# Kernel tuning notes

Measured on AMD Instinct MI355X. Metric: run time of the kernel, lower is better.

The kernel has to match this reference:

```python
import jax, jax.numpy as jnp
import numpy as np

EMBED_DIM = 1024
NUM_HEADS = 16
HEAD_DIM = EMBED_DIM // NUM_HEADS
SCALING = HEAD_DIM ** -0.5
TGT_LEN, BSZ = 2048, 2


def setup_inputs() -> dict:
    key = jax.random.key(0)
    k1, k2, k3 = jax.random.split(key, 3)
    return {
        "query": jax.random.normal(k1, (TGT_LEN, BSZ, EMBED_DIM), jnp.float32),
        "in_proj_weight": jax.random.normal(k2, (3 * EMBED_DIM, EMBED_DIM), jnp.float32) * (EMBED_DIM ** -0.5),
        "in_proj_bias": jnp.zeros((3 * EMBED_DIM,), jnp.float32),
        "out_w": jax.random.normal(k3, (EMBED_DIM, EMBED_DIM), jnp.float32) * (EMBED_DIM ** -0.5),
        "out_b": jnp.zeros((EMBED_DIM,), jnp.float32),
    }


def reference(query, in_proj_weight, in_proj_bias, out_w, out_b):
    tgt_len, bsz, embed_dim = query.shape
    # fused QKV projection (self-attention path: qkv_same)
    qkv = query @ in_proj_weight.T + in_proj_bias  # [T, B, 3E]
    q, k, v = jnp.split(qkv, 3, axis=-1)
    q = q * SCALING
    # [T, B, E] -> [B*H, T, hd]
    def to_heads(x):
        return x.reshape(tgt_len, bsz * NUM_HEADS, HEAD_DIM).transpose(1, 0, 2)
    q, k, v = to_heads(q), to_heads(k), to_heads(v)
    attn_weights = jnp.einsum('bqd,bkd->bqk', q, k)          # [B*H, T, T]
    attn_weights = jax.nn.softmax(attn_weights, axis=-1)
    attn = jnp.einsum('bqk,bkd->bqd', attn_weights, v)       # [B*H, T, hd]
    attn = attn.transpose(1, 0, 2).reshape(tgt_len, bsz, embed_dim)
    attn = attn @ out_w.T + out_b
    # averaged attention weights over heads (need_weights=True)
    avg_weights = attn_weights.reshape(bsz, NUM_HEADS, tgt_len, tgt_len).mean(axis=1)
    return attn, avg_weights
```

## Files before the change

### kernel.cpp

```cpp
#include <hip/hip_runtime.h>
#include <hip/hip_bf16.h>
#include <math.h>

#define T_LEN 2048
#define BSZ   2
#define EMB   1024
#define NH    16
#define HD    64
#define BHN   (BSZ*NH)
#define M1    (T_LEN*BSZ)
#define SCAL  0.125f
#define QSCALE (0.125f * 1.44269504088896f)

typedef __attribute__((ext_vector_type(8))) short bf16x8;
typedef __attribute__((ext_vector_type(4))) float f32x4;
typedef __attribute__((ext_vector_type(2))) unsigned int u32x2;

__device__ inline unsigned short f2bf(float x) {
    union { float f; unsigned u; } v; v.f = x;
    unsigned r = v.u + 0x7FFF + ((v.u >> 16) & 1);
    return (unsigned short)(r >> 16);
}

__device__ inline unsigned pack2bf(float a, float b) {
    union { __hip_bfloat162 h; unsigned u; } v;
    v.h = __float22bfloat162_rn(make_float2(a, b));
    return v.u;
}

__device__ inline float fexp2(float x) {
#if __has_builtin(__builtin_amdgcn_exp2f)
    return __builtin_amdgcn_exp2f(x);
#else
    return exp2f(x);
#endif
}

__device__ inline void async16(const unsigned short* g, unsigned short* l) {
    __builtin_amdgcn_global_load_lds(
        (const __attribute__((address_space(1))) void*)g,
        (__attribute__((address_space(3))) void*)l, 16, 0, 0);
}

__device__ inline void bar() {
    asm volatile("" ::: "memory");
    __builtin_amdgcn_s_barrier();
    asm volatile("" ::: "memory");
}

__device__ inline const unsigned short* swz(const unsigned short* base, int r, int c) {
    return base + (((r << 3) + (c ^ (r & 7))) << 3);
}
__device__ inline const unsigned short* swz16(const unsigned short* base, int r, int c) {
    return base + (((r << 4) + (c ^ (r & 7))) << 3);
}

__device__ inline void xchg(unsigned e, unsigned o, unsigned& w_lo, unsigned& w_hi) {
#if __has_builtin(__builtin_amdgcn_permlane32_swap) && __has_builtin(__builtin_amdgcn_permlane16_swap)
    u32x2 x = __builtin_amdgcn_permlane32_swap(e, o, false, false);
    u32x2 y = __builtin_amdgcn_permlane16_swap(x[0], x[1], false, false);
    w_lo = y[0]; w_hi = y[1];
#else
    int lane = (int)(threadIdx.x & 63);
    int quad = lane >> 4, l16 = lane & 15;
    int srcA = ((quad & 1) * 2) * 16 + l16;
    int srcB = ((quad & 1) * 2 + 1) * 16 + l16;
    unsigned ea = (unsigned)__shfl((int)e, srcA, 64);
    unsigned oa = (unsigned)__shfl((int)o, srcA, 64);
    unsigned eb = (unsigned)__shfl((int)e, srcB, 64);
    unsigned ob = (unsigned)__shfl((int)o, srcB, 64);
    w_lo = (quad >> 1) ? oa : ea;
    w_hi = (quad >> 1) ? ob : eb;
#endif
}

__global__ __launch_bounds__(256) void cvt3_kernel(
    const float* __restrict__ s0, const float* __restrict__ s1,
    const float* __restrict__ s2, unsigned short* __restrict__ dst,
    int n0, int n1)
{
    int idx = blockIdx.x * 256 + threadIdx.x;
    const float* src; int o;
    if (idx < n0)           { src = s0; o = idx; }
    else if (idx < n0 + n1) { src = s1; o = idx - n0; }
    else                    { src = s2; o = idx - n0 - n1; }
    float4 a = reinterpret_cast<const float4*>(src)[(size_t)o * 2];
    float4 c = reinterpret_cast<const float4*>(src)[(size_t)o * 2 + 1];
    unsigned w[4] = { pack2bf(a.x, a.y), pack2bf(a.z, a.w),
                      pack2bf(c.x, c.y), pack2bf(c.z, c.w) };
    reinterpret_cast<uint4*>(dst)[idx] = *reinterpret_cast<uint4*>(w);
}

__global__ __launch_bounds__(256) void qkv_mfma_kernel(
    const unsigned short* __restrict__ A, const unsigned short* __restrict__ B,
    const float* __restrict__ bias,
    unsigned short* __restrict__ Q16, unsigned short* __restrict__ K16,
    unsigned short* __restrict__ Vt16)
{
    constexpr int BM = 128, BN = 128, BK = 32, K = 1024;
    __shared__ unsigned short As[BM * BK];
    __shared__ unsigned short Bs[BN * BK];
    const int tid = threadIdx.x;
    const int lane = tid & 63, wave = tid >> 6;
    const int quad = lane >> 4, l16 = lane & 15;
    const int wr = wave >> 1, wc = wave & 1;
    const int m0 = blockIdx.x * BM, n0 = blockIdx.y * BN;

    f32x4 zero4 = {0.f, 0.f, 0.f, 0.f};
    f32x4 acc[4][4];
    #pragma unroll
    for (int i = 0; i < 4; ++i)
        #pragma unroll
        for (int j = 0; j < 4; ++j) acc[i][j] = zero4;

    for (int k0 = 0; k0 < K; k0 += BK) {
        __syncthreads();
        #pragma unroll
        for (int t = 0; t < 2; ++t) {
            int c = t * 256 + tid;
            int m = c >> 2, kb = c & 3;
            async16(&A[(size_t)(m0 + m) * K + k0 + kb * 8], &As[c * 8]);
            async16(&B[(size_t)(n0 + m) * K + k0 + kb * 8], &Bs[c * 8]);
        }
        __syncthreads();
        bf16x8 af[4], bfr[4];
        #pragma unroll
        for (int i = 0; i < 4; ++i) {
            af[i]  = *reinterpret_cast<const bf16x8*>(&As[(wr * 64 + i * 16 + l16) * BK + quad * 8]);
            bfr[i] = *reinterpret_cast<const bf16x8*>(&Bs[(wc * 64 + i * 16 + l16) * BK + quad * 8]);
        }
        #pragma unroll
        for (int i = 0; i < 4; ++i)
            #pragma unroll
            for (int j = 0; j < 4; ++j)
                acc[i][j] = __builtin_amdgcn_mfma_f32_16x16x32_bf16(af[i], bfr[j], acc[i][j], 0, 0, 0);
    }

    #pragma unroll
    for (int j = 0; j < 4; ++j) {
        int n = n0 + wc * 64 + j * 16 + l16;
        float bv = bias[n];
        int which = n >> 10;
        int c = n & 1023;
        int h = c >> 6, d = c & 63;
        #pragma unroll
        for (int i = 0; i < 4; ++i) {
            #pragma unroll
            for (int r = 0; r < 4; ++r) {
                int m = m0 + wr * 64 + i * 16 + quad * 4 + r;
                int t = m >> 1, b = m & 1;
                int bh = b * NH + h;
                float v = acc[i][j][r] + bv;
                if (which == 0)      Q16[((size_t)bh * T_LEN + t) * HD + d] = f2bf(v * QSCALE);
                else if (which == 1) K16[((size_t)bh * T_LEN + t) * HD + d] = f2bf(v);
                else                 Vt16[((size_t)bh * HD + d) * T_LEN + t] = f2bf(v);
            }
        }
    }
}

__global__ __launch_bounds__(512, 4) void flash_mfma_kernel(
    const unsigned short* __restrict__ Qb, const unsigned short* __restrict__ Kb,
    const unsigned short* __restrict__ Vt, unsigned short* __restrict__ AO,
    float* __restrict__ Rrow)
{
    __shared__ unsigned short Ks[2][128 * 64];
    __shared__ unsigned short Vs[2][64 * 128];
    const int tid = threadIdx.x;
    const int lane = tid & 63, wave = tid >> 6;
    const int quad = lane >> 4, l16 = lane & 15;

    const int lin = blockIdx.y * gridDim.x + blockIdx.x;
    const int xcd = lin & 7, slot = lin >> 3;
    const int bh = xcd * 4 + (slot >> 4);
    const int qt = slot & 15;
    const int q0 = qt * 128;
    const int b = bh >> 4, h = bh & 15;

    const unsigned short* Qp =
        Qb + ((size_t)bh * T_LEN + q0 + wave * 16 + l16) * HD;
    bf16x8 qf0 = *reinterpret_cast<const bf16x8*>(Qp + quad * 8);
    bf16x8 qf1 = *reinterpret_cast<const bf16x8*>(Qp + 32 + quad * 8);

    f32x4 zero4 = {0.f, 0.f, 0.f, 0.f};
    f32x4 oacc[4] = {zero4, zero4, zero4, zero4};
    float l_part = 0.f;

    const unsigned short* Kbase = Kb + (size_t)bh * T_LEN * HD;
    const unsigned short* Vbase = Vt + (size_t)bh * HD * T_LEN;

    const int ck0 = tid, ck1 = tid + 512;
    const int kr0 = ck0 >> 3, kc0 = (ck0 & 7) ^ (kr0 & 7);
    const int kr1 = ck1 >> 3, kc1 = (ck1 & 7) ^ (kr1 & 7);
    const int vr0 = ck0 >> 4, vc0 = (ck0 & 15) ^ (vr0 & 7);
    const int vr1 = ck1 >> 4, vc1 = (ck1 & 15) ^ (vr1 & 7);

    auto stage = [&](int buf, int kt) {
        async16(&Kbase[(size_t)(kt + kr0) * HD + kc0 * 8], &Ks[buf][ck0 * 8]);
        async16(&Kbase[(size_t)(kt + kr1) * HD + kc1 * 8], &Ks[buf][ck1 * 8]);
        async16(&Vbase[(size_t)vr0 * T_LEN + kt + vc0 * 8], &Vs[buf][ck0 * 8]);
        async16(&Vbase[(size_t)vr1 * T_LEN + kt + vc1 * 8], &Vs[buf][ck1 * 8]);
    };

    stage(0, 0);

    int cur = 0;
    for (int kt = 0; kt < T_LEN; kt += 128) {
        if (kt + 128 < T_LEN) {
            stage(cur ^ 1, kt + 128);
            asm volatile("s_waitcnt vmcnt(4)" ::: "memory");
        } else {
            asm volatile("s_waitcnt vmcnt(0)" ::: "memory");
        }
        bar();

        const unsigned short* Kt = Ks[cur];
        const unsigned short* Vv = Vs[cur];

        unsigned dlo[8], dhi[8];
        #pragma unroll
        for (int half = 0; half < 2; ++half) {
            f32x4 sacc[4] = {zero4, zero4, zero4, zero4};
            __builtin_amdgcn_s_setprio(1);
            #pragma unroll
            for (int j = 0; j < 4; ++j) {
                int kb = half * 4 + j;
                bf16x8 kf0 = *reinterpret_cast<const bf16x8*>(swz(Kt, kb * 16 + l16, quad));
                sacc[j] = __builtin_amdgcn_mfma_f32_16x16x32_bf16(kf0, qf0, sacc[j], 0, 0, 0);
                bf16x8 kf1 = *reinterpret_cast<const bf16x8*>(swz(Kt, kb * 16 + l16, 4 + quad));
                sacc[j] = __builtin_amdgcn_mfma_f32_16x16x32_bf16(kf1, qf1, sacc[j], 0, 0, 0);
            }
            __builtin_amdgcn_s_setprio(0);
            #pragma unroll
            for (int j = 0; j < 4; ++j) {
                float p0 = fexp2(sacc[j][0]);
                float p1 = fexp2(sacc[j][1]);
                float p2 = fexp2(sacc[j][2]);
                float p3 = fexp2(sacc[j][3]);
                l_part += (p0 + p1) + (p2 + p3);
                dlo[half * 4 + j] = pack2bf(p0, p1);
                dhi[half * 4 + j] = pack2bf(p2, p3);
            }
        }

        __builtin_amdgcn_s_setprio(1);
        #pragma unroll
        for (int ks = 0; ks < 4; ++ks) {
            unsigned w0, w1, w2, w3;
            xchg(dlo[2 * ks], dlo[2 * ks + 1], w0, w2);
            xchg(dhi[2 * ks], dhi[2 * ks + 1], w1, w3);
            union { bf16x8 v; unsigned u[4]; } P;
            P.u[0] = w0; P.u[1] = w1; P.u[2] = w2; P.u[3] = w3;
            #pragma unroll
            for (int dt = 0; dt < 4; ++dt) {
                bf16x8 va = *reinterpret_cast<const bf16x8*>(swz16(Vv, dt * 16 + l16, ks * 4 + quad));
                oacc[dt] = __builtin_amdgcn_mfma_f32_16x16x32_bf16(va, P.v, oacc[dt], 0, 0, 0);
            }
        }
        __builtin_amdgcn_s_setprio(0);

        bar();
        cur ^= 1;
    }

    l_part += __shfl_xor(l_part, 16);
    l_part += __shfl_xor(l_part, 32);
    float rl = 1.0f / l_part;
    int q = q0 + wave * 16 + l16;
    size_t base = ((size_t)q * BSZ + b) * EMB + h * HD;
    #pragma unroll
    for (int dt = 0; dt < 4; ++dt) {
        unsigned o[2] = { pack2bf(oacc[dt][0] * rl, oacc[dt][1] * rl),
                          pack2bf(oacc[dt][2] * rl, oacc[dt][3] * rl) };
        *reinterpret_cast<uint2*>(&AO[base + dt * 16 + quad * 4]) = *reinterpret_cast<uint2*>(o);
    }
    if (quad == 0)
        Rrow[(size_t)bh * T_LEN + q] = rl;
}

__global__ __launch_bounds__(256) void avg_mfma_kernel(
    const unsigned short* __restrict__ Qb, const unsigned short* __restrict__ Kb,
    const float* __restrict__ Rrow, float* __restrict__ avg_out)
{
    __shared__ unsigned short Ks[2][2][64 * 64];
    const int tid = threadIdx.x;
    const int lane = tid & 63, wave = tid >> 6;
    const int quad = lane >> 4, l16 = lane & 15;
    const int kt = blockIdx.x, qt = blockIdx.y, b = blockIdx.z;
    const int q0 = qt * 128, k0 = kt * 64;

    auto stage_pair = [&](int buf, int h0) {
        const unsigned short* Kg = Kb + ((size_t)(b * NH + h0) * T_LEN + k0) * HD;
        #pragma unroll
        for (int t = 0; t < 4; ++t) {
            int c = t * 256 + tid;
            int hh = c >> 9, cl = c & 511;
            int r = cl >> 3, cc = (cl & 7) ^ (r & 7);
            async16(&Kg[(size_t)hh * T_LEN * HD + (size_t)r * HD + cc * 8],
                    &Ks[buf][0][0] + (size_t)c * 8);
        }
    };

    f32x4 zero4 = {0.f, 0.f, 0.f, 0.f};
    f32x4 acc[2][4];
    #pragma unroll
    for (int s = 0; s < 2; ++s)
        #pragma unroll
        for (int c = 0; c < 4; ++c) acc[s][c] = zero4;

    stage_pair(0, 0);
    int cur = 0;
    for (int g = 0; g < NH / 2; ++g) {
        if (g + 1 < NH / 2) {
            stage_pair(cur ^ 1, 2 * (g + 1));
            asm volatile("s_waitcnt vmcnt(4)" ::: "memory");
        } else {
            asm volatile("s_waitcnt vmcnt(0)" ::: "memory");
        }
        bar();

        #pragma unroll
        for (int hh = 0; hh < 2; ++hh) {
            const int bh = b * NH + 2 * g + hh;
            const unsigned short* Kt = Ks[cur][hh];
            bf16x8 kf[4][2];
            #pragma unroll
            for (int c = 0; c < 4; ++c) {
                kf[c][0] = *reinterpret_cast<const bf16x8*>(swz(Kt, c * 16 + l16, quad));
                kf[c][1] = *reinterpret_cast<const bf16x8*>(swz(Kt, c * 16 + l16, 4 + quad));
            }
            #pragma unroll
            for (int s = 0; s < 2; ++s) {
                const int qrow = q0 + s * 64 + wave * 16;
                const unsigned short* Qp = Qb + ((size_t)bh * T_LEN + qrow + l16) * HD;
                bf16x8 qf0 = *reinterpret_cast<const bf16x8*>(Qp + quad * 8);
                bf16x8 qf1 = *reinterpret_cast<const bf16x8*>(Qp + 32 + quad * 8);
                float4 rlv = *reinterpret_cast<const float4*>(
                    &Rrow[(size_t)bh * T_LEN + qrow + quad * 4]);

                f32x4 sacc[4] = {zero4, zero4, zero4, zero4};
                __builtin_amdgcn_s_setprio(1);
                #pragma unroll
                for (int c = 0; c < 4; ++c) {
                    sacc[c] = __builtin_amdgcn_mfma_f32_16x16x32_bf16(qf0, kf[c][0], sacc[c], 0, 0, 0);
                    sacc[c] = __builtin_amdgcn_mfma_f32_16x16x32_bf16(qf1, kf[c][1], sacc[c], 0, 0, 0);
                }
                __builtin_amdgcn_s_setprio(0);

                float rl4[4] = { rlv.x, rlv.y, rlv.z, rlv.w };
                #pragma unroll
                for (int c = 0; c < 4; ++c)
                    #pragma unroll
                    for (int r = 0; r < 4; ++r)
                        acc[s][c][r] += fexp2(sacc[c][r]) * rl4[r];
            }
        }
        bar();
        cur ^= 1;
    }

    #pragma unroll
    for (int s = 0; s < 2; ++s)
        #pragma unroll
        for (int r = 0; r < 4; ++r) {
            int q = q0 + s * 64 + wave * 16 + quad * 4 + r;
            size_t base = ((size_t)b * T_LEN + q) * T_LEN + k0;
            #pragma unroll
            for (int c = 0; c < 4; ++c)
                avg_out[base + c * 16 + l16] = acc[s][c][r] * (1.0f / 16.0f);
        }
}

__global__ __launch_bounds__(256) void out_mfma_kernel(
    const unsigned short* __restrict__ A, const unsigned short* __restrict__ B,
    const float* __restrict__ bias, float* __restrict__ out)
{
    constexpr int BM = 128, BN = 128, BK = 32, K = 1024;
    __shared__ unsigned short As[BM * BK];
    __shared__ unsigned short Bs[BN * BK];
    const int tid = threadIdx.x;
    const int lane = tid & 63, wave = tid >> 6;
    const int quad = lane >> 4, l16 = lane & 15;
    const int wr = wave >> 1, wc = wave & 1;
    const int m0 = blockIdx.x * BM, n0 = blockIdx.y * BN;

    f32x4 zero4 = {0.f, 0.f, 0.f, 0.f};
    f32x4 acc[4][4];
    #pragma unroll
    for (int i = 0; i < 4; ++i)
        #pragma unroll
        for (int j = 0; j < 4; ++j) acc[i][j] = zero4;

    for (int k0 = 0; k0 < K; k0 += BK) {
        __syncthreads();
        #pragma unroll
        for (int t = 0; t < 2; ++t) {
            int c = t * 256 + tid;
            int m = c >> 2, kb = c & 3;
            async16(&A[(size_t)(m0 + m) * K + k0 + kb * 8], &As[c * 8]);
            async16(&B[(size_t)(n0 + m) * K + k0 + kb * 8], &Bs[c * 8]);
        }
        __syncthreads();
        bf16x8 af[4], bfr[4];
        #pragma unroll
        for (int i = 0; i < 4; ++i) {
            af[i]  = *reinterpret_cast<const bf16x8*>(&As[(wr * 64 + i * 16 + l16) * BK + quad * 8]);
            bfr[i] = *reinterpret_cast<const bf16x8*>(&Bs[(wc * 64 + i * 16 + l16) * BK + quad * 8]);
        }
        #pragma unroll
        for (int i = 0; i < 4; ++i)
            #pragma unroll
            for (int j = 0; j < 4; ++j)
                acc[i][j] = __builtin_amdgcn_mfma_f32_16x16x32_bf16(af[i], bfr[j], acc[i][j], 0, 0, 0);
    }

    #pragma unroll
    for (int j = 0; j < 4; ++j) {
        int n = n0 + wc * 64 + j * 16 + l16;
        float bv = bias[n];
        #pragma unroll
        for (int i = 0; i < 4; ++i) {
            #pragma unroll
            for (int r = 0; r < 4; ++r) {
                int m = m0 + wr * 64 + i * 16 + quad * 4 + r;
                out[(size_t)m * 1024 + n] = acc[i][j][r] + bv;
            }
        }
    }
}

extern "C" void kernel_launch(void* const* d_in, const int* in_sizes, int n_in,
                              void* d_out, int out_size, void* d_ws, size_t ws_size,
                              hipStream_t stream)
{
    const float* query = (const float*)d_in[0];
    const float* wqkv  = (const float*)d_in[1];
    const float* bqkv  = (const float*)d_in[2];
    const float* wout  = (const float*)d_in[3];
    const float* bout  = (const float*)d_in[4];
    float* out = (float*)d_out;

    char* ws = (char*)d_ws;
    const size_t E_Q   = (size_t)M1 * EMB;
    const size_t E_W   = (size_t)3 * EMB * EMB;
    const size_t E_WO  = (size_t)EMB * EMB;
    const size_t E_QKV = (size_t)BHN * T_LEN * HD;

    unsigned short* queryb = (unsigned short*)ws;
    unsigned short* wqkvb  = queryb + E_Q;
    unsigned short* woutb  = wqkvb + E_W;
    unsigned short* Q16    = woutb + E_WO;
    unsigned short* K16    = Q16 + E_QKV;
    unsigned short* Vt16   = K16 + E_QKV;
    unsigned short* AO16   = Vt16 + E_QKV;
    float* Lr = (float*)(AO16 + E_Q);
    const size_t need = (E_Q + E_W + E_WO + 4 * E_QKV) * 2 + (size_t)BHN * T_LEN * 4;
    if (ws_size < need) return;

    cvt3_kernel<<<(int)((E_Q + E_W + E_WO) / 8 / 256), 256, 0, stream>>>(
        query, wqkv, wout, queryb, (int)(E_Q / 8), (int)(E_W / 8));

    qkv_mfma_kernel<<<dim3(M1 / 128, 3072 / 128), 256, 0, stream>>>(queryb, wqkvb, bqkv, Q16, K16, Vt16);
    flash_mfma_kernel<<<dim3(T_LEN / 128, BHN), 512, 0, stream>>>(Q16, K16, Vt16, AO16, Lr);
    avg_mfma_kernel<<<dim3(T_LEN / 64, T_LEN / 128, BSZ), 256, 0, stream>>>(Q16, K16, Lr, out + (size_t)M1 * EMB);
    out_mfma_kernel<<<dim3(M1 / 128, 1024 / 128), 256, 0, stream>>>(AO16, woutb, bout, out);
}
```

Measured before the change: 240.6 us.

## Load K fragments directly to registers in avg kernel, dropping LDS staging

The head-averaged attention-weights kernel no longer stages K tiles through shared memory with async copies and barriers. Each wave now loads its K MFMA fragments straight from global memory into registers, double-buffered in registers across heads so the next head's load overlaps the current head's compute. This removes LDS traffic and block-wide synchronisation, but every wave now fetches the same K data redundantly from global/L2, and register pressure rises from the two fragment buffers.

```diff
diff --git a/kernel.cpp b/kernel.cpp
--- a/kernel.cpp
+++ b/kernel.cpp
@@ -282,25 +282,12 @@
     const unsigned short* __restrict__ Qb, const unsigned short* __restrict__ Kb,
     const float* __restrict__ Rrow, float* __restrict__ avg_out)
 {
-    __shared__ unsigned short Ks[2][2][64 * 64];
     const int tid = threadIdx.x;
     const int lane = tid & 63, wave = tid >> 6;
     const int quad = lane >> 4, l16 = lane & 15;
     const int kt = blockIdx.x, qt = blockIdx.y, b = blockIdx.z;
     const int q0 = qt * 128, k0 = kt * 64;
 
-    auto stage_pair = [&](int buf, int h0) {
-        const unsigned short* Kg = Kb + ((size_t)(b * NH + h0) * T_LEN + k0) * HD;
-        #pragma unroll
-        for (int t = 0; t < 4; ++t) {
-            int c = t * 256 + tid;
-            int hh = c >> 9, cl = c & 511;
-            int r = cl >> 3, cc = (cl & 7) ^ (r & 7);
-            async16(&Kg[(size_t)hh * T_LEN * HD + (size_t)r * HD + cc * 8],
-                    &Ks[buf][0][0] + (size_t)c * 8);
-        }
-    };
-
     f32x4 zero4 = {0.f, 0.f, 0.f, 0.f};
     f32x4 acc[2][4];
     #pragma unroll
@@ -308,55 +295,56 @@
         #pragma unroll
         for (int c = 0; c < 4; ++c) acc[s][c] = zero4;
 
-    stage_pair(0, 0);
-    int cur = 0;
+    const unsigned short* Kl =
+        Kb + ((size_t)(b * NH) * T_LEN + k0 + l16) * HD + quad * 8;
+
+    auto loadK = [&](bf16x8 (&kf)[4][2], int h) {
+        const unsigned short* p = Kl + (size_t)h * T_LEN * HD;
+        #pragma unroll
+        for (int c = 0; c < 4; ++c) {
+            kf[c][0] = *reinterpret_cast<const bf16x8*>(p + (size_t)c * 16 * HD);
+            kf[c][1] = *reinterpret_cast<const bf16x8*>(p + (size_t)c * 16 * HD + 32);
+        }
+    };
+
+    auto compute = [&](bf16x8 (&kf)[4][2], int h) {
+        const int bh = b * NH + h;
+        #pragma unroll
+        for (int s = 0; s < 2; ++s) {
+            const int qrow = q0 + s * 64 + wave * 16;
+            const unsigned short* Qp = Qb + ((size_t)bh * T_LEN + qrow + l16) * HD;
+            bf16x8 qf0 = *reinterpret_cast<const bf16x8*>(Qp + quad * 8);
+            bf16x8 qf1 = *reinterpret_cast<const bf16x8*>(Qp + 32 + quad * 8);
+            float4 rlv = *reinterpret_cast<const float4*>(
+                &Rrow[(size_t)bh * T_LEN + qrow + quad * 4]);
+
+            f32x4 sacc[4] = {zero4, zero4, zero4, zero4};
+            __builtin_amdgcn_s_setprio(1);
+            #pragma unroll
+            for (int c = 0; c < 4; ++c) {
+                sacc[c] = __builtin_amdgcn_mfma_f32_16x16x32_bf16(qf0, kf[c][0], sacc[c], 0, 0, 0);
+                sacc[c] = __builtin_amdgcn_mfma_f32_16x16x32_bf16(qf1, kf[c][1], sacc[c], 0, 0, 0);
+            }
+            __builtin_amdgcn_s_setprio(0);
+
+            float rl4[4] = { rlv.x, rlv.y, rlv.z, rlv.w };
+            #pragma unroll
+            for (int c = 0; c < 4; ++c)
+                #pragma unroll
+                for (int r = 0; r < 4; ++r)
+                    acc[s][c][r] += fexp2(sacc[c][r]) * rl4[r];
+        }
+    };
+
+    bf16x8 kfA[4][2], kfB[4][2];
+    loadK(kfA, 0);
+    #pragma unroll
     for (int g = 0; g < NH / 2; ++g) {
-        if (g + 1 < NH / 2) {
-            stage_pair(cur ^ 1, 2 * (g + 1));
-            asm volatile("s_waitcnt vmcnt(4)" ::: "memory");
-        } else {
-            asm volatile("s_waitcnt vmcnt(0)" ::: "memory");
-        }
-        bar();
-
-        #pragma unroll
-        for (int hh = 0; hh < 2; ++hh) {
-            const int bh = b * NH + 2 * g + hh;
-            const unsigned short* Kt = Ks[cur][hh];
-            bf16x8 kf[4][2];
-            #pragma unroll
-            for (int c = 0; c < 4; ++c) {
-                kf[c][0] = *reinterpret_cast<const bf16x8*>(swz(Kt, c * 16 + l16, quad));
-                kf[c][1] = *reinterpret_cast<const bf16x8*>(swz(Kt, c * 16 + l16, 4 + quad));
-            }
-            #pragma unroll
-            for (int s = 0; s < 2; ++s) {
-                const int qrow = q0 + s * 64 + wave * 16;
-                const unsigned short* Qp = Qb + ((size_t)bh * T_LEN + qrow + l16) * HD;
-                bf16x8 qf0 = *reinterpret_cast<const bf16x8*>(Qp + quad * 8);
-                bf16x8 qf1 = *reinterpret_cast<const bf16x8*>(Qp + 32 + quad * 8);
-                float4 rlv = *reinterpret_cast<const float4*>(
-                    &Rrow[(size_t)bh * T_LEN + qrow + quad * 4]);
-
-                f32x4 sacc[4] = {zero4, zero4, zero4, zero4};
-                __builtin_amdgcn_s_setprio(1);
-                #pragma unroll
-                for (int c = 0; c < 4; ++c) {
-                    sacc[c] = __builtin_amdgcn_mfma_f32_16x16x32_bf16(qf0, kf[c][0], sacc[c], 0, 0, 0);
-                    sacc[c] = __builtin_amdgcn_mfma_f32_16x16x32_bf16(qf1, kf[c][1], sacc[c], 0, 0, 0);
-                }
-                __builtin_amdgcn_s_setprio(0);
-
-                float rl4[4] = { rlv.x, rlv.y, rlv.z, rlv.w };
-                #pragma unroll
-                for (int c = 0; c < 4; ++c)
-                    #pragma unroll
-                    for (int r = 0; r < 4; ++r)
-                        acc[s][c][r] += fexp2(sacc[c][r]) * rl4[r];
-            }
-        }
-        bar();
-        cur ^= 1;
+        loadK(kfB, 2 * g + 1);
+        compute(kfA, 2 * g);
+        if (2 * g + 2 < NH)
+            loadK(kfA, 2 * g + 2);
+        compute(kfB, 2 * g + 1);
     }
 
     #pragma unroll
```

After: 333.0 us. +38.4%, slower.

## Merge averaged-weights and output-projection kernels into one interleaved launch

Applied to the files above, without the earlier changes.

Combines the head-averaged attention weight kernel and the output projection GEMM into a single launch of 1280 blocks, where every fifth block runs a GEMM tile and the rest run avg tiles, sharing one shared-memory buffer. This removes one kernel launch and the tail/idle gap between the two kernels, letting the compute-heavy GEMM tiles overlap with the store-heavy avg tiles. The cost is a larger register and shared-memory footprint taken as the maximum of both paths, which may lower occupancy, plus block-level divergence in scheduling.

```diff
diff --git a/kernel.cpp b/kernel.cpp
--- a/kernel.cpp
+++ b/kernel.cpp
@@ -278,154 +278,153 @@
         Rrow[(size_t)bh * T_LEN + q] = rl;
 }
 
-__global__ __launch_bounds__(256) void avg_mfma_kernel(
+__global__ __launch_bounds__(256) void avgout_kernel(
     const unsigned short* __restrict__ Qb, const unsigned short* __restrict__ Kb,
-    const float* __restrict__ Rrow, float* __restrict__ avg_out)
+    const float* __restrict__ Rrow, float* __restrict__ avg_out,
+    const unsigned short* __restrict__ A, const unsigned short* __restrict__ B,
+    const float* __restrict__ bias, float* __restrict__ out)
 {
-    __shared__ unsigned short Ks[2][2][64 * 64];
+    __shared__ __align__(16) unsigned short smem[16384];
     const int tid = threadIdx.x;
     const int lane = tid & 63, wave = tid >> 6;
     const int quad = lane >> 4, l16 = lane & 15;
-    const int kt = blockIdx.x, qt = blockIdx.y, b = blockIdx.z;
-    const int q0 = qt * 128, k0 = kt * 64;
-
-    auto stage_pair = [&](int buf, int h0) {
-        const unsigned short* Kg = Kb + ((size_t)(b * NH + h0) * T_LEN + k0) * HD;
-        #pragma unroll
-        for (int t = 0; t < 4; ++t) {
-            int c = t * 256 + tid;
-            int hh = c >> 9, cl = c & 511;
-            int r = cl >> 3, cc = (cl & 7) ^ (r & 7);
-            async16(&Kg[(size_t)hh * T_LEN * HD + (size_t)r * HD + cc * 8],
-                    &Ks[buf][0][0] + (size_t)c * 8);
-        }
-    };
-
+    const int gid = blockIdx.x;
+    const int g5 = gid / 5, r5 = gid - g5 * 5;
     f32x4 zero4 = {0.f, 0.f, 0.f, 0.f};
-    f32x4 acc[2][4];
-    #pragma unroll
-    for (int s = 0; s < 2; ++s)
-        #pragma unroll
-        for (int c = 0; c < 4; ++c) acc[s][c] = zero4;
-
-    stage_pair(0, 0);
-    int cur = 0;
-    for (int g = 0; g < NH / 2; ++g) {
-        if (g + 1 < NH / 2) {
-            stage_pair(cur ^ 1, 2 * (g + 1));
-            asm volatile("s_waitcnt vmcnt(4)" ::: "memory");
-        } else {
-            asm volatile("s_waitcnt vmcnt(0)" ::: "memory");
-        }
-        bar();
-
-        #pragma unroll
-        for (int hh = 0; hh < 2; ++hh) {
-            const int bh = b * NH + 2 * g + hh;
-            const unsigned short* Kt = Ks[cur][hh];
-            bf16x8 kf[4][2];
-            #pragma unroll
-            for (int c = 0; c < 4; ++c) {
-                kf[c][0] = *reinterpret_cast<const bf16x8*>(swz(Kt, c * 16 + l16, quad));
-                kf[c][1] = *reinterpret_cast<const bf16x8*>(swz(Kt, c * 16 + l16, 4 + quad));
-            }
-            #pragma unroll
-            for (int s = 0; s < 2; ++s) {
-                const int qrow = q0 + s * 64 + wave * 16;
-                const unsigned short* Qp = Qb + ((size_t)bh * T_LEN + qrow + l16) * HD;
-                bf16x8 qf0 = *reinterpret_cast<const bf16x8*>(Qp + quad * 8);
-                bf16x8 qf1 = *reinterpret_cast<const bf16x8*>(Qp + 32 + quad * 8);
-                float4 rlv = *reinterpret_cast<const float4*>(
-                    &Rrow[(size_t)bh * T_LEN + qrow + quad * 4]);
-
-                f32x4 sacc[4] = {zero4, zero4, zero4, zero4};
-                __builtin_amdgcn_s_setprio(1);
+
+    if (r5 == 4) {
+        constexpr int BM = 128, BN = 128, BK = 32, K = 1024;
+        unsigned short* As = smem;
+        unsigned short* Bs = smem + 4096;
+        const int wr = wave >> 1, wc = wave & 1;
+        const int m0 = (g5 & 31) * BM, n0 = (g5 >> 5) * BN;
+
+        f32x4 acc[4][4];
+        #pragma unroll
+        for (int i = 0; i < 4; ++i)
+            #pragma unroll
+            for (int j = 0; j < 4; ++j) acc[i][j] = zero4;
+
+        for (int k0 = 0; k0 < K; k0 += BK) {
+            __syncthreads();
+            #pragma unroll
+            for (int t = 0; t < 2; ++t) {
+                int c = t * 256 + tid;
+                int m = c >> 2, kb = c & 3;
+                async16(&A[(size_t)(m0 + m) * K + k0 + kb * 8], &As[c * 8]);
+                async16(&B[(size_t)(n0 + m) * K + k0 + kb * 8], &Bs[c * 8]);
+            }
+            __syncthreads();
+            bf16x8 af[4], bfr[4];
+            #pragma unroll
+            for (int i = 0; i < 4; ++i) {
+                af[i]  = *reinterpret_cast<const bf16x8*>(&As[(wr * 64 + i * 16 + l16) * BK + quad * 8]);
+                bfr[i] = *reinterpret_cast<const bf16x8*>(&Bs[(wc * 64 + i * 16 + l16) * BK + quad * 8]);
+            }
+            #pragma unroll
+            for (int i = 0; i < 4; ++i)
+                #pragma unroll
+                for (int j = 0; j < 4; ++j)
+                    acc[i][j] = __builtin_amdgcn_mfma_f32_16x16x32_bf16(af[i], bfr[j], acc[i][j], 0, 0, 0);
+        }
+
+        #pragma unroll
+        for (int j = 0; j < 4; ++j) {
+            int n = n0 + wc * 64 + j * 16 + l16;
+            float bv = bias[n];
+            #pragma unroll
+            for (int i = 0; i < 4; ++i) {
+                #pragma unroll
+                for (int r = 0; r < 4; ++r) {
+                    int m = m0 + wr * 64 + i * 16 + quad * 4 + r;
+                    out[(size_t)m * 1024 + n] = acc[i][j][r] + bv;
+                }
+            }
+        }
+    } else {
+        const int ai = g5 * 4 + r5;
+        const int kt = ai & 31, qt = (ai >> 5) & 15, b = ai >> 9;
+        const int q0 = qt * 128, k0 = kt * 64;
+
+        auto stage_pair = [&](int buf, int h0) {
+            const unsigned short* Kg = Kb + ((size_t)(b * NH + h0) * T_LEN + k0) * HD;
+            #pragma unroll
+            for (int t = 0; t < 4; ++t) {
+                int c = t * 256 + tid;
+                int hh = c >> 9, cl = c & 511;
+                int r = cl >> 3, cc = (cl & 7) ^ (r & 7);
+                async16(&Kg[(size_t)hh * T_LEN * HD + (size_t)r * HD + cc * 8],
+                        smem + buf * 8192 + (size_t)c * 8);
+            }
+        };
+
+        f32x4 acc[2][4];
+        #pragma unroll
+        for (int s = 0; s < 2; ++s)
+            #pragma unroll
+            for (int c = 0; c < 4; ++c) acc[s][c] = zero4;
+
+        stage_pair(0, 0);
+        int cur = 0;
+        for (int g = 0; g < NH / 2; ++g) {
+            if (g + 1 < NH / 2) {
+                stage_pair(cur ^ 1, 2 * (g + 1));
+                asm volatile("s_waitcnt vmcnt(4)" ::: "memory");
+            } else {
+                asm volatile("s_waitcnt vmcnt(0)" ::: "memory");
+            }
+            bar();
+
+            #pragma unroll
+            for (int hh = 0; hh < 2; ++hh) {
+                const int bh = b * NH + 2 * g + hh;
+                const unsigned short* Kt = smem + cur * 8192 + hh * 4096;
+                bf16x8 kf[4][2];
                 #pragma unroll
                 for (int c = 0; c < 4; ++c) {
-                    sacc[c] = __builtin_amdgcn_mfma_f32_16x16x32_bf16(qf0, kf[c][0], sacc[c], 0, 0, 0);
-                    sacc[c] = __builtin_amdgcn_mfma_f32_16x16x32_bf16(qf1, kf[c][1], sacc[c], 0, 0, 0);
+                    kf[c][0] = *reinterpret_cast<const bf16x8*>(swz(Kt, c * 16 + l16, quad));
+                    kf[c][1] = *reinterpret_cast<const bf16x8*>(swz(Kt, c * 16 + l16, 4 + quad));
                 }
-                __builtin_amdgcn_s_setprio(0);
-
-                float rl4[4] = { rlv.x, rlv.y, rlv.z, rlv.w };
+                #pragma unroll
+                for (int s = 0; s < 2; ++s) {
+                    const int qrow = q0 + s * 64 + wave * 16;
+                    const unsigned short* Qp = Qb + ((size_t)bh * T_LEN + qrow + l16) * HD;
+                    bf16x8 qf0 = *reinterpret_cast<const bf16x8*>(Qp + quad * 8);
+                    bf16x8 qf1 = *reinterpret_cast<const bf16x8*>(Qp + 32 + quad * 8);
+                    float4 rlv = *reinterpret_cast<const float4*>(
+                        &Rrow[(size_t)bh * T_LEN + qrow + quad * 4]);
+
+                    f32x4 sacc[4] = {zero4, zero4, zero4, zero4};
+                    __builtin_amdgcn_s_setprio(1);
+                    #pragma unroll
+                    for (int c = 0; c < 4; ++c) {
+                        sacc[c] = __builtin_amdgcn_mfma_f32_16x16x32_bf16(qf0, kf[c][0], sacc[c], 0, 0, 0);
+                        sacc[c] = __builtin_amdgcn_mfma_f32_16x16x32_bf16(qf1, kf[c][1], sacc[c], 0, 0, 0);
+                    }
+                    __builtin_amdgcn_s_setprio(0);
+
+                    float rl4[4] = { rlv.x, rlv.y, rlv.z, rlv.w };
+                    #pragma unroll
+                    for (int c = 0; c < 4; ++c)
+                        #pragma unroll
+                        for (int r = 0; r < 4; ++r)
+                            acc[s][c][r] += fexp2(sacc[c][r]) * rl4[r];
+                }
+            }
+            bar();
+            cur ^= 1;
+        }
+
+        #pragma unroll
+        for (int s = 0; s < 2; ++s)
+            #pragma unroll
+            for (int r = 0; r < 4; ++r) {
+                int q = q0 + s * 64 + wave * 16 + quad * 4 + r;
+                size_t base = ((size_t)b * T_LEN + q) * T_LEN + k0;
                 #pragma unroll
                 for (int c = 0; c < 4; ++c)
-                    #pragma unroll
-                    for (int r = 0; r < 4; ++r)
-                        acc[s][c][r] += fexp2(sacc[c][r]) * rl4[r];
-            }
-        }
-        bar();
-        cur ^= 1;
-    }
-
-    #pragma unroll
-    for (int s = 0; s < 2; ++s)
-        #pragma unroll
-        for (int r = 0; r < 4; ++r) {
-            int q = q0 + s * 64 + wave * 16 + quad * 4 + r;
-            size_t base = ((size_t)b * T_LEN + q) * T_LEN + k0;
-            #pragma unroll
-            for (int c = 0; c < 4; ++c)
-                avg_out[base + c * 16 + l16] = acc[s][c][r] * (1.0f / 16.0f);
-        }
-}
-
-__global__ __launch_bounds__(256) void out_mfma_kernel(
-    const unsigned short* __restrict__ A, const unsigned short* __restrict__ B,
-    const float* __restrict__ bias, float* __restrict__ out)
-{
-    constexpr int BM = 128, BN = 128, BK = 32, K = 1024;
-    __shared__ unsigned short As[BM * BK];
-    __shared__ unsigned short Bs[BN * BK];
-    const int tid = threadIdx.x;
-    const int lane = tid & 63, wave = tid >> 6;
-    const int quad = lane >> 4, l16 = lane & 15;
-    const int wr = wave >> 1, wc = wave & 1;
-    const int m0 = blockIdx.x * BM, n0 = blockIdx.y * BN;
-
-    f32x4 zero4 = {0.f, 0.f, 0.f, 0.f};
-    f32x4 acc[4][4];
-    #pragma unroll
-    for (int i = 0; i < 4; ++i)
-        #pragma unroll
-        for (int j = 0; j < 4; ++j) acc[i][j] = zero4;
-
-    for (int k0 = 0; k0 < K; k0 += BK) {
-        __syncthreads();
-        #pragma unroll
-        for (int t = 0; t < 2; ++t) {
-            int c = t * 256 + tid;
-            int m = c >> 2, kb = c & 3;
-            async16(&A[(size_t)(m0 + m) * K + k0 + kb * 8], &As[c * 8]);
-            async16(&B[(size_t)(n0 + m) * K + k0 + kb * 8], &Bs[c * 8]);
-        }
-        __syncthreads();
-        bf16x8 af[4], bfr[4];
-        #pragma unroll
-        for (int i = 0; i < 4; ++i) {
-            af[i]  = *reinterpret_cast<const bf16x8*>(&As[(wr * 64 + i * 16 + l16) * BK + quad * 8]);
-            bfr[i] = *reinterpret_cast<const bf16x8*>(&Bs[(wc * 64 + i * 16 + l16) * BK + quad * 8]);
-        }
-        #pragma unroll
-        for (int i = 0; i < 4; ++i)
-            #pragma unroll
-            for (int j = 0; j < 4; ++j)
-                acc[i][j] = __builtin_amdgcn_mfma_f32_16x16x32_bf16(af[i], bfr[j], acc[i][j], 0, 0, 0);
-    }
-
-    #pragma unroll
-    for (int j = 0; j < 4; ++j) {
-        int n = n0 + wc * 64 + j * 16 + l16;
-        float bv = bias[n];
-        #pragma unroll
-        for (int i = 0; i < 4; ++i) {
-            #pragma unroll
-            for (int r = 0; r < 4; ++r) {
-                int m = m0 + wr * 64 + i * 16 + quad * 4 + r;
-                out[(size_t)m * 1024 + n] = acc[i][j][r] + bv;
-            }
-        }
+                    avg_out[base + c * 16 + l16] = acc[s][c][r] * (1.0f / 16.0f);
+            }
     }
 }
 
@@ -462,6 +461,6 @@
 
     qkv_mfma_kernel<<<dim3(M1 / 128, 3072 / 128), 256, 0, stream>>>(queryb, wqkvb, bqkv, Q16, K16, Vt16);
     flash_mfma_kernel<<<dim3(T_LEN / 128, BHN), 512, 0, stream>>>(Q16, K16, Vt16, AO16, Lr);
-    avg_mfma_kernel<<<dim3(T_LEN / 64, T_LEN / 128, BSZ), 256, 0, stream>>>(Q16, K16, Lr, out + (size_t)M1 * EMB);
-    out_mfma_kernel<<<dim3(M1 / 128, 1024 / 128), 256, 0, stream>>>(AO16, woutb, bout, out);
-}
+    avgout_kernel<<<1280, 256, 0, stream>>>(Q16, K16, Lr, out + (size_t)M1 * EMB,
+                                            AO16, woutb, bout, out);
+}
```

Result: no change. 238.8 us (-0.8%).
